# Kernel tuning notes

Measured on AMD Instinct MI355X. Metric: run time of the kernel, lower is better.

Reference implementation:

```python
import jax, jax.numpy as jnp
import numpy as np

PAD = 0
SIGMA_C = 2.0
EPS = 1e-6
LOG_SQRT_2PI = 0.9189385332046727  # log(sqrt(2*pi))

B, T_CHAR, VOCAB, D_EMB = 32, 256, 100, 384


def setup_inputs() -> dict:
    rng = np.random.default_rng(0)
    # text tokens in [1, VOCAB): avoid pad (=0) inside the utterance
    text = rng.integers(1, VOCAB, size=(B, T_CHAR), dtype=np.int64)
    # per-char durations in frames, 1..8
    durs = rng.integers(1, 9, size=(B, T_CHAR), dtype=np.int32)
    # total_time = length of repeat_interleave(text, durs) padded to batch max
    total_time = int(durs.sum(axis=-1).max())
    key = jax.random.key(0)
    embed = jax.random.normal(key, (VOCAB, D_EMB), dtype=jnp.float32)
    return {
        "text": jnp.asarray(text),
        "durs": jnp.asarray(durs),
        "embed": embed,
        "total_time": total_time,
    }


def reference(text, durs, embed, total_time):
    # Pad 2 trailing positions: pad token, zero duration (as in the original)
    text = jnp.pad(text, ((0, 0), (0, 2)), constant_values=PAD)      # [B, Tc]
    durs = jnp.pad(durs, ((0, 0), (0, 2)), constant_values=0)        # [B, Tc]
    durs_f = durs.astype(jnp.float32)

    # Gaussian centers: mid-point of each char's frame span
    csum = jnp.cumsum(durs_f, axis=-1)
    c = durs_f / 2.0 + jnp.pad(csum[:, :-1], ((0, 0), (1, 0)))       # [B, Tc]
    sig = durs_f / SIGMA_C + EPS                                     # [B, Tc]

    t = jnp.arange(total_time, dtype=jnp.float32) + 0.5              # [Tt]

    # Gaussian pdf evaluated at frame times: w[b, t, c]
    z = (t[None, :, None] - c[:, None, :]) / sig[:, None, :]         # [B, Tt, Tc]
    w = jnp.exp(-0.5 * z * z - jnp.log(sig)[:, None, :] - LOG_SQRT_2PI)

    # zero padded-char columns, normalize over chars
    char_pad = (text == PAD)[:, None, :]                             # [B, 1, Tc]
    w = jnp.where(char_pad, 0.0, w)
    w = w / (jnp.sum(w, axis=-1, keepdims=True) + EPS)

    # time positions past each utterance's total duration are padding:
    # zero the whole row, then put weight 1.0 on the last (pad) char column
    total_dur = jnp.sum(durs, axis=-1)                               # [B]
    time_pad = jnp.arange(total_time)[None, :] >= total_dur[:, None] # [B, Tt]
    w = jnp.where(time_pad[:, :, None], 0.0, w)
    w = w.at[:, :, -1].set(jnp.where(time_pad, 1.0, w[:, :, -1]))

    # aggregate gathered embeddings: [B, Tt, Tc] x [B, Tc, D] -> [B, Tt, D]
    u = jnp.einsum("btc,bcd->btd", w, embed[text])
    return u
```

## Files before the change

### kernel.cpp

```cpp
#include <hip/hip_runtime.h>

#define TC 256
#define DEMB 384
#define WIN 96
#define TTILE 32
#define LOG_SQRT_2PI 0.9189385332046727f

__global__ __launch_bounds__(256) void gauss_embed_kernel(
    const int* __restrict__ text,
    const int* __restrict__ durs,
    const float* __restrict__ embed,
    float* __restrict__ out,
    int Tt)
{
    const int b   = blockIdx.y;
    const int t0  = blockIdx.x * TTILE;
    const int tid = threadIdx.x;

    __shared__ float s_scan[TC];
    __shared__ float s_wc[WIN], s_wis[WIN], s_wA[WIN];
    __shared__ int   s_wtx[WIN];
    __shared__ __align__(16) float s_w[WIN][TTILE];
    __shared__ float s_invS[TTILE];
    __shared__ int   s_j0, s_totdur;

    s_scan[tid] = (float)durs[b * TC + tid];
    if (tid == 0) s_j0 = TC - 1;
    __syncthreads();
    for (int ofs = 1; ofs < TC; ofs <<= 1) {
        float v = (tid >= ofs) ? s_scan[tid - ofs] : 0.0f;
        __syncthreads();
        s_scan[tid] += v;
        __syncthreads();
    }

    {
        int en = (int)s_scan[tid];
        int st = tid ? (int)s_scan[tid - 1] : 0;
        if (t0 >= st && t0 < en) s_j0 = tid;
        if (tid == 0) s_totdur = (int)s_scan[TC - 1];
    }
    __syncthreads();

    int base = s_j0 - 31;
    base = base < 0 ? 0 : (base > TC - WIN ? TC - WIN : base);
    const int totdur = s_totdur;

    if (tid < WIN) {
        int j = base + tid;
        float endf   = s_scan[j];
        float startf = j ? s_scan[j - 1] : 0.0f;
        float dur = endf - startf;
        float sig = dur * 0.5f + 1e-6f;
        s_wc[tid]  = endf - dur * 0.5f;
        s_wis[tid] = 1.0f / sig;
        s_wA[tid]  = -logf(sig) - LOG_SQRT_2PI;
        s_wtx[tid] = text[b * TC + j];
    }
    __syncthreads();

    for (int i = tid; i < WIN * TTILE; i += 256) {
        int c  = i >> 5;
        int tt = i & 31;
        float tf = (float)(t0 + tt) + 0.5f;
        float z  = (tf - s_wc[c]) * s_wis[c];
        float p  = fmaf(-0.5f * z, z, s_wA[c]);
        s_w[c][tt] = expf(p);
    }
    __syncthreads();

    if (tid < TTILE) {
        float s = 0.0f;
        for (int c = 0; c < WIN; ++c) s += s_w[c][tid];
        s_invS[tid] = 1.0f / (s + 1e-6f);
    }
    __syncthreads();

    const int wv   = tid >> 6;
    const int lane = tid & 63;
    const int tb   = wv * 8;

    float2 acc[8][3];
#pragma unroll
    for (int i = 0; i < 8; ++i)
#pragma unroll
        for (int k = 0; k < 3; ++k) acc[i][k] = make_float2(0.0f, 0.0f);

    for (int c = 0; c < WIN; ++c) {
        int idx = __builtin_amdgcn_readfirstlane(s_wtx[c]);
        const float2* erow = (const float2*)(embed + (size_t)idx * DEMB);
        float2 e0 = erow[lane];
        float2 e1 = erow[lane + 64];
        float2 e2 = erow[lane + 128];
        const float4 wa = *(const float4*)(&s_w[c][tb]);
        const float4 wb = *(const float4*)(&s_w[c][tb + 4]);
        float wl[8] = {wa.x, wa.y, wa.z, wa.w, wb.x, wb.y, wb.z, wb.w};
#pragma unroll
        for (int tt = 0; tt < 8; ++tt) {
            float wgt = wl[tt];
            acc[tt][0].x = fmaf(wgt, e0.x, acc[tt][0].x);
            acc[tt][0].y = fmaf(wgt, e0.y, acc[tt][0].y);
            acc[tt][1].x = fmaf(wgt, e1.x, acc[tt][1].x);
            acc[tt][1].y = fmaf(wgt, e1.y, acc[tt][1].y);
            acc[tt][2].x = fmaf(wgt, e2.x, acc[tt][2].x);
            acc[tt][2].y = fmaf(wgt, e2.y, acc[tt][2].y);
        }
    }

    const float2* prow = (const float2*)embed;
    float2 p0 = prow[lane], p1 = prow[lane + 64], p2 = prow[lane + 128];

#pragma unroll
    for (int tt = 0; tt < 8; ++tt) {
        int t = t0 + tb + tt;
        if (t >= Tt) continue;
        float2 o0, o1, o2;
        if (t >= totdur) {
            o0 = p0; o1 = p1; o2 = p2;
        } else {
            float s = s_invS[tb + tt];
            o0 = make_float2(acc[tt][0].x * s, acc[tt][0].y * s);
            o1 = make_float2(acc[tt][1].x * s, acc[tt][1].y * s);
            o2 = make_float2(acc[tt][2].x * s, acc[tt][2].y * s);
        }
        float2* orow = (float2*)(out + (size_t)(b * Tt + t) * DEMB);
        orow[lane]       = o0;
        orow[lane + 64]  = o1;
        orow[lane + 128] = o2;
    }
}

extern "C" void kernel_launch(void* const* d_in, const int* in_sizes, int n_in,
                              void* d_out, int out_size, void* d_ws, size_t ws_size,
                              hipStream_t stream) {
    const int*   text  = (const int*)d_in[0];
    const int*   durs  = (const int*)d_in[1];
    const float* embed = (const float*)d_in[2];
    float* out = (float*)d_out;

    const int B = 32;
    const int Tt = out_size / (B * DEMB);

    dim3 grid((Tt + TTILE - 1) / TTILE, B);
    gauss_embed_kernel<<<grid, 256, 0, stream>>>(text, durs, embed, out, Tt);
}
```

Baseline: 125.4 us.

## Halve block threads, give each wave 16 time rows, pair-scan durations

Blocks drop from 256 to 128 threads, so each wave now accumulates 16 time rows instead of 8. Each embedding row load is therefore reused across twice as many outputs, and fewer waves per block fetch the same window rows. The prefix scan is reworked so each thread sums a pair of durations and then rebuilds the per-char cumulative sums, which keeps the scan correct with half the threads. The cost is twice the accumulator registers per thread and fewer waves per block, which may cut occupancy and latency hiding.

```diff
diff --git a/kernel.cpp b/kernel.cpp
--- a/kernel.cpp
+++ b/kernel.cpp
@@ -4,9 +4,10 @@
 #define DEMB 384
 #define WIN 96
 #define TTILE 32
+#define NTHR 128
 #define LOG_SQRT_2PI 0.9189385332046727f
 
-__global__ __launch_bounds__(256) void gauss_embed_kernel(
+__global__ __launch_bounds__(NTHR, 2) void gauss_embed_kernel(
     const int* __restrict__ text,
     const int* __restrict__ durs,
     const float* __restrict__ embed,
@@ -18,26 +19,39 @@
     const int tid = threadIdx.x;
 
     __shared__ float s_scan[TC];
+    __shared__ float s_pair[NTHR];
     __shared__ float s_wc[WIN], s_wis[WIN], s_wA[WIN];
     __shared__ int   s_wtx[WIN];
     __shared__ __align__(16) float s_w[WIN][TTILE];
     __shared__ float s_invS[TTILE];
     __shared__ int   s_j0, s_totdur;
 
-    s_scan[tid] = (float)durs[b * TC + tid];
+    const int dA = durs[b * TC + 2 * tid];
+    const int dB = durs[b * TC + 2 * tid + 1];
+    s_pair[tid] = (float)(dA + dB);
     if (tid == 0) s_j0 = TC - 1;
     __syncthreads();
-    for (int ofs = 1; ofs < TC; ofs <<= 1) {
-        float v = (tid >= ofs) ? s_scan[tid - ofs] : 0.0f;
+    for (int ofs = 1; ofs < NTHR; ofs <<= 1) {
+        float v = (tid >= ofs) ? s_pair[tid - ofs] : 0.0f;
         __syncthreads();
-        s_scan[tid] += v;
+        s_pair[tid] += v;
         __syncthreads();
     }
+    {
+        float P = s_pair[tid];
+        s_scan[2 * tid + 1] = P;
+        s_scan[2 * tid]     = P - (float)dB;
+    }
+    __syncthreads();
 
     {
-        int en = (int)s_scan[tid];
-        int st = tid ? (int)s_scan[tid - 1] : 0;
-        if (t0 >= st && t0 < en) s_j0 = tid;
+#pragma unroll
+        for (int k = 0; k < 2; ++k) {
+            int j  = 2 * tid + k;
+            int en = (int)s_scan[j];
+            int st = j ? (int)s_scan[j - 1] : 0;
+            if (t0 >= st && t0 < en) s_j0 = j;
+        }
         if (tid == 0) s_totdur = (int)s_scan[TC - 1];
     }
     __syncthreads();
@@ -59,7 +73,7 @@
     }
     __syncthreads();
 
-    for (int i = tid; i < WIN * TTILE; i += 256) {
+    for (int i = tid; i < WIN * TTILE; i += NTHR) {
         int c  = i >> 5;
         int tt = i & 31;
         float tf = (float)(t0 + tt) + 0.5f;
@@ -78,25 +92,29 @@
 
     const int wv   = tid >> 6;
     const int lane = tid & 63;
-    const int tb   = wv * 8;
+    const int tb   = wv * 16;
 
-    float2 acc[8][3];
+    float2 acc[16][3];
 #pragma unroll
-    for (int i = 0; i < 8; ++i)
+    for (int i = 0; i < 16; ++i)
 #pragma unroll
         for (int k = 0; k < 3; ++k) acc[i][k] = make_float2(0.0f, 0.0f);
 
+#pragma unroll 2
     for (int c = 0; c < WIN; ++c) {
         int idx = __builtin_amdgcn_readfirstlane(s_wtx[c]);
         const float2* erow = (const float2*)(embed + (size_t)idx * DEMB);
         float2 e0 = erow[lane];
         float2 e1 = erow[lane + 64];
         float2 e2 = erow[lane + 128];
-        const float4 wa = *(const float4*)(&s_w[c][tb]);
-        const float4 wb = *(const float4*)(&s_w[c][tb + 4]);
-        float wl[8] = {wa.x, wa.y, wa.z, wa.w, wb.x, wb.y, wb.z, wb.w};
+        const float4 w0 = *(const float4*)(&s_w[c][tb]);
+        const float4 w1 = *(const float4*)(&s_w[c][tb + 4]);
+        const float4 w2 = *(const float4*)(&s_w[c][tb + 8]);
+        const float4 w3 = *(const float4*)(&s_w[c][tb + 12]);
+        float wl[16] = {w0.x, w0.y, w0.z, w0.w, w1.x, w1.y, w1.z, w1.w,
+                        w2.x, w2.y, w2.z, w2.w, w3.x, w3.y, w3.z, w3.w};
 #pragma unroll
-        for (int tt = 0; tt < 8; ++tt) {
+        for (int tt = 0; tt < 16; ++tt) {
             float wgt = wl[tt];
             acc[tt][0].x = fmaf(wgt, e0.x, acc[tt][0].x);
             acc[tt][0].y = fmaf(wgt, e0.y, acc[tt][0].y);
@@ -111,7 +129,7 @@
     float2 p0 = prow[lane], p1 = prow[lane + 64], p2 = prow[lane + 128];
 
 #pragma unroll
-    for (int tt = 0; tt < 8; ++tt) {
+    for (int tt = 0; tt < 16; ++tt) {
         int t = t0 + tb + tt;
         if (t >= Tt) continue;
         float2 o0, o1, o2;
@@ -142,5 +160,5 @@
     const int Tt = out_size / (B * DEMB);
 
     dim3 grid((Tt + TTILE - 1) / TTILE, B);
-    gauss_embed_kernel<<<grid, 256, 0, stream>>>(text, durs, embed, out, Tt);
+    gauss_embed_kernel<<<grid, NTHR, 0, stream>>>(text, durs, embed, out, Tt);
 }
```

Result: faster. 118.1 us (-5.9%).

## Use bf16 MFMA for weighted embedding sum with LDS-staged transposed table

Applied to the files above, without the earlier changes.

Adds a pre-pass that transposes the embedding table to bf16 in workspace, then stages the whole table into LDS through direct global-to-LDS loads in each block. The Gaussian weights are computed per time step in bf16, and the window-by-embedding contraction runs on 16x16x32 bf16 MFMA instead of scalar FMAs, with B operands gathered from LDS by token index. This targets the FP32 FMA throughput and the repeated global embedding row reads. In exchange it lowers precision to bf16, launches an extra kernel, and uses about 80KB of LDS per block, which may reduce occupancy.

```diff
diff --git a/kernel.cpp b/kernel.cpp
--- a/kernel.cpp
+++ b/kernel.cpp
@@ -2,26 +2,52 @@
 
 #define TC 256
 #define DEMB 384
+#define VOC 100
 #define WIN 96
 #define TTILE 32
+#define WPS 104
 #define LOG_SQRT_2PI 0.9189385332046727f
 
-__global__ __launch_bounds__(256) void gauss_embed_kernel(
+typedef short v8s __attribute__((ext_vector_type(8)));
+typedef float v4f __attribute__((ext_vector_type(4)));
+
+__device__ __forceinline__ unsigned short f32_to_bf16_rne(float f) {
+    union { float f; unsigned int u; } x; x.f = f;
+    unsigned int u = x.u;
+    return (unsigned short)((u + 0x7FFFu + ((u >> 16) & 1u)) >> 16);
+}
+
+__global__ __launch_bounds__(256) void embed_transpose_kernel(
+    const float* __restrict__ embed, unsigned short* __restrict__ embT)
+{
+    int i = blockIdx.x * 256 + threadIdx.x;
+    if (i >= DEMB * VOC) return;
+    int n = i / VOC, v = i - n * VOC;
+    embT[i] = f32_to_bf16_rne(embed[v * DEMB + n]);
+}
+
+__global__ __launch_bounds__(256) void gauss_embed_mfma_kernel(
     const int* __restrict__ text,
     const int* __restrict__ durs,
     const float* __restrict__ embed,
+    const unsigned short* __restrict__ embT,
     float* __restrict__ out,
     int Tt)
 {
     const int b   = blockIdx.y;
     const int t0  = blockIdx.x * TTILE;
     const int tid = threadIdx.x;
+    const int wv   = tid >> 6;
+    const int lane = tid & 63;
+    const int nq   = lane & 15;
+    const int q    = lane >> 4;
 
+    __shared__ __align__(16) unsigned short s_embT[DEMB * VOC];
+    __shared__ __align__(16) unsigned short s_wp[TTILE * WPS];
     __shared__ float s_scan[TC];
-    __shared__ float s_wc[WIN], s_wis[WIN], s_wA[WIN];
+    __shared__ float s_part[256];
+    __shared__ float s_invS[TTILE];
     __shared__ int   s_wtx[WIN];
-    __shared__ __align__(16) float s_w[WIN][TTILE];
-    __shared__ float s_invS[TTILE];
     __shared__ int   s_j0, s_totdur;
 
     s_scan[tid] = (float)durs[b * TC + tid];
@@ -46,87 +72,96 @@
     base = base < 0 ? 0 : (base > TC - WIN ? TC - WIN : base);
     const int totdur = s_totdur;
 
-    if (tid < WIN) {
-        int j = base + tid;
-        float endf   = s_scan[j];
-        float startf = j ? s_scan[j - 1] : 0.0f;
-        float dur = endf - startf;
-        float sig = dur * 0.5f + 1e-6f;
-        s_wc[tid]  = endf - dur * 0.5f;
-        s_wis[tid] = 1.0f / sig;
-        s_wA[tid]  = -logf(sig) - LOG_SQRT_2PI;
-        s_wtx[tid] = text[b * TC + j];
+    {
+        const char* gsrc = (const char*)embT;
+        for (int ch = wv; ch < 75; ch += 4) {
+            __builtin_amdgcn_global_load_lds(
+                (const __attribute__((address_space(1))) unsigned int*)(gsrc + ch * 1024 + lane * 16),
+                (__attribute__((address_space(3))) unsigned int*)((char*)s_embT + ch * 1024),
+                16, 0, 0);
+        }
     }
-    __syncthreads();
 
-    for (int i = tid; i < WIN * TTILE; i += 256) {
-        int c  = i >> 5;
-        int tt = i & 31;
-        float tf = (float)(t0 + tt) + 0.5f;
-        float z  = (tf - s_wc[c]) * s_wis[c];
-        float p  = fmaf(-0.5f * z, z, s_wA[c]);
-        s_w[c][tt] = expf(p);
+    {
+        const int t = tid & 31;
+        const int g = tid >> 5;
+        const float tf = (float)(t0 + t) + 0.5f;
+        float lsum = 0.0f;
+#pragma unroll
+        for (int cc = 0; cc < 12; ++cc) {
+            int c = g * 12 + cc;
+            int j = base + c;
+            float endf   = s_scan[j];
+            float startf = j ? s_scan[j - 1] : 0.0f;
+            float dur = endf - startf;
+            float sig = dur * 0.5f + 1e-6f;
+            float ctr = endf - dur * 0.5f;
+            float z = (tf - ctr) / sig;
+            float w = __expf(fmaf(-0.5f * z, z, -__logf(sig) - LOG_SQRT_2PI));
+            lsum += w;
+            s_wp[t * WPS + c] = f32_to_bf16_rne(w);
+        }
+        s_part[tid] = lsum;
+        if (tid < WIN) s_wtx[tid] = text[b * TC + base + tid];
     }
     __syncthreads();
 
     if (tid < TTILE) {
-        float s = 0.0f;
-        for (int c = 0; c < WIN; ++c) s += s_w[c][tid];
-        s_invS[tid] = 1.0f / (s + 1e-6f);
+        float s = 1e-6f;
+#pragma unroll
+        for (int g = 0; g < 8; ++g) s += s_part[g * 32 + tid];
+        s_invS[tid] = 1.0f / s;
     }
     __syncthreads();
 
-    const int wv   = tid >> 6;
-    const int lane = tid & 63;
-    const int tb   = wv * 8;
+    v4f acc[6][2];
+#pragma unroll
+    for (int nt = 0; nt < 6; ++nt)
+#pragma unroll
+        for (int mt = 0; mt < 2; ++mt) {
+            v4f z = {0.0f, 0.0f, 0.0f, 0.0f};
+            acc[nt][mt] = z;
+        }
 
-    float2 acc[8][3];
 #pragma unroll
-    for (int i = 0; i < 8; ++i)
+    for (int ks = 0; ks < 3; ++ks) {
+        const int c0 = ks * 32;
+        int vidx[8];
 #pragma unroll
-        for (int k = 0; k < 3; ++k) acc[i][k] = make_float2(0.0f, 0.0f);
-
-    for (int c = 0; c < WIN; ++c) {
-        int idx = __builtin_amdgcn_readfirstlane(s_wtx[c]);
-        const float2* erow = (const float2*)(embed + (size_t)idx * DEMB);
-        float2 e0 = erow[lane];
-        float2 e1 = erow[lane + 64];
-        float2 e2 = erow[lane + 128];
-        const float4 wa = *(const float4*)(&s_w[c][tb]);
-        const float4 wb = *(const float4*)(&s_w[c][tb + 4]);
-        float wl[8] = {wa.x, wa.y, wa.z, wa.w, wb.x, wb.y, wb.z, wb.w};
+        for (int j = 0; j < 8; ++j) vidx[j] = s_wtx[c0 + q * 8 + j];
+        v8s a0 = *(const v8s*)(s_wp + nq * WPS + c0 + q * 8);
+        v8s a1 = *(const v8s*)(s_wp + (16 + nq) * WPS + c0 + q * 8);
 #pragma unroll
-        for (int tt = 0; tt < 8; ++tt) {
-            float wgt = wl[tt];
-            acc[tt][0].x = fmaf(wgt, e0.x, acc[tt][0].x);
-            acc[tt][0].y = fmaf(wgt, e0.y, acc[tt][0].y);
-            acc[tt][1].x = fmaf(wgt, e1.x, acc[tt][1].x);
-            acc[tt][1].y = fmaf(wgt, e1.y, acc[tt][1].y);
-            acc[tt][2].x = fmaf(wgt, e2.x, acc[tt][2].x);
-            acc[tt][2].y = fmaf(wgt, e2.y, acc[tt][2].y);
+        for (int nt = 0; nt < 6; ++nt) {
+            const unsigned short* col = s_embT + (wv * 96 + nt * 16 + nq) * VOC;
+            v8s bf;
+#pragma unroll
+            for (int j = 0; j < 8; ++j) bf[j] = (short)col[vidx[j]];
+            acc[nt][0] = __builtin_amdgcn_mfma_f32_16x16x32_bf16(a0, bf, acc[nt][0], 0, 0, 0);
+            acc[nt][1] = __builtin_amdgcn_mfma_f32_16x16x32_bf16(a1, bf, acc[nt][1], 0, 0, 0);
         }
     }
 
-    const float2* prow = (const float2*)embed;
-    float2 p0 = prow[lane], p1 = prow[lane + 64], p2 = prow[lane + 128];
+    float pe[6];
+#pragma unroll
+    for (int nt = 0; nt < 6; ++nt) pe[nt] = embed[wv * 96 + nt * 16 + nq];
 
 #pragma unroll
-    for (int tt = 0; tt < 8; ++tt) {
-        int t = t0 + tb + tt;
-        if (t >= Tt) continue;
-        float2 o0, o1, o2;
-        if (t >= totdur) {
-            o0 = p0; o1 = p1; o2 = p2;
-        } else {
-            float s = s_invS[tb + tt];
-            o0 = make_float2(acc[tt][0].x * s, acc[tt][0].y * s);
-            o1 = make_float2(acc[tt][1].x * s, acc[tt][1].y * s);
-            o2 = make_float2(acc[tt][2].x * s, acc[tt][2].y * s);
+    for (int mt = 0; mt < 2; ++mt) {
+#pragma unroll
+        for (int r = 0; r < 4; ++r) {
+            int tl = mt * 16 + q * 4 + r;
+            int t = t0 + tl;
+            if (t >= Tt) continue;
+            float sv = s_invS[tl];
+            bool pad = (t >= totdur);
+            float* orow = out + (size_t)(b * Tt + t) * DEMB + wv * 96 + nq;
+#pragma unroll
+            for (int nt = 0; nt < 6; ++nt) {
+                float val = pad ? pe[nt] : acc[nt][mt][r] * sv;
+                orow[nt * 16] = val;
+            }
         }
-        float2* orow = (float2*)(out + (size_t)(b * Tt + t) * DEMB);
-        orow[lane]       = o0;
-        orow[lane + 64]  = o1;
-        orow[lane + 128] = o2;
     }
 }
 
@@ -141,6 +176,9 @@
     const int B = 32;
     const int Tt = out_size / (B * DEMB);
 
+    unsigned short* embT = (unsigned short*)d_ws;
+    embed_transpose_kernel<<<(DEMB * VOC + 255) / 256, 256, 0, stream>>>(embed, embT);
+
     dim3 grid((Tt + TTILE - 1) / TTILE, B);
-    gauss_embed_kernel<<<grid, 256, 0, stream>>>(text, durs, embed, out, Tt);
+    gauss_embed_mfma_kernel<<<grid, 256, 0, stream>>>(text, durs, embed, embT, out, Tt);
 }
```

Result: faster. 106.0 us (-15.5%).
